# Performance work log

Measured on AMD Instinct MI355X. Metric: run time of the kernel, lower is better.

## Reference

```python
import jax, jax.numpy as jnp
import numpy as np

HIDDEN = 512


def setup_inputs() -> dict:
    key = jax.random.key(0)
    k_x, k_ih, k_hh = jax.random.split(key, 3)
    B, T, I, H = 128, 1000, 2, HIDDEN
    x = jax.random.uniform(k_x, (B, T, I), dtype=jnp.float32)
    s_ih = 1.0 / np.sqrt(I)
    s_hh = 1.0 / np.sqrt(H)
    weight_ih = jax.random.normal(k_ih, (I, 4 * H), dtype=jnp.float32) * s_ih
    weight_hh = jax.random.normal(k_hh, (H, 4 * H), dtype=jnp.float32) * s_hh
    bias = jnp.zeros((4 * H,), dtype=jnp.float32)
    return {"x": x, "weight_ih": weight_ih, "weight_hh": weight_hh, "bias": bias}


def _lstm(x, weight_ih, weight_hh, bias):
    # x: [B, T, I] (batch_first) -> scan over time
    B, T, I = x.shape
    H = weight_hh.shape[0]
    # Precompute input contribution for all timesteps: [T, B, 4H]
    x_t = jnp.transpose(x, (1, 0, 2))
    xW = jnp.einsum('tbi,ih->tbh', x_t, weight_ih) + bias

    def step(carry, xw_t):
        h0, c0 = carry
        gates = h0 @ weight_hh + xw_t  # [B, 4H]
        f, i, o, g = jnp.split(gates, 4, axis=1)
        c1 = jax.nn.sigmoid(f) * c0 + jax.nn.sigmoid(i) * jnp.tanh(g)
        h1 = jax.nn.sigmoid(o) * jnp.tanh(c1)
        return (h1, c1), (h1, c1)

    h0 = jnp.zeros((B, H), dtype=x.dtype)
    c0 = jnp.zeros((B, H), dtype=x.dtype)
    _, (h_n, c_n) = jax.lax.scan(step, (h0, c0), xW)
    # [T, B, H] -> [B, T, H] (batch_first)
    return jnp.transpose(h_n, (1, 0, 2)), jnp.transpose(c_n, (1, 0, 2))


def reference(x, weight_ih, weight_hh, bias):
    return _lstm(x, weight_ih, weight_hh, bias)
```

## Files before the change

### kernel.cpp

```cpp
#include <hip/hip_runtime.h>

#define TT 1000
#define HH 512
#define G4 2048
#define NG 32
#define SLOTS 8
#define SPG 4
#define HCBLK 64

typedef __attribute__((ext_vector_type(8))) short bf16x8;
typedef __attribute__((ext_vector_type(4))) float f32x4;

__device__ __forceinline__ float sigm(float v) { return 1.0f / (1.0f + __expf(-v)); }
__device__ __forceinline__ float tanh_fast(float v) { return 2.0f / (1.0f + __expf(-2.0f * v)) - 1.0f; }

__device__ __forceinline__ unsigned short bf16rne(float f) {
    unsigned u = __float_as_uint(f);
    return (unsigned short)((u + 0x7fffu + ((u >> 16) & 1u)) >> 16);
}

__global__ __launch_bounds__(512, 1)
void lstm_bo(const float* __restrict__ x,
             const float* __restrict__ wih,
             const float* __restrict__ whh,
             const float* __restrict__ bias,
             float* __restrict__ out,
             float* ws)
{
    __shared__ unsigned long long ldsA[2][4][132];

    const int bid  = blockIdx.x;
    const int g    = bid & (NG - 1);
    const int slot = bid >> 5;
    const int tid  = threadIdx.x;
    const int wv   = tid >> 6;
    const int lane = tid & 63;
    const int col  = lane & 15;
    const int kb   = lane >> 4;
    const int q    = col & 3;
    const int q1   = q & 1, q2 = q >> 1;
    const int cc   = col >> 2;
    const int hc0  = slot * HCBLK + wv * 8 + cc;
    const int hc1  = hc0 + 4;

    unsigned long long* slab = (unsigned long long*)ws;
    unsigned* flags = (unsigned*)((char*)ws + 256 * 1024);

    for (int i = tid; i < 2 * 4 * 132; i += 512)
        ((unsigned long long*)ldsA)[i] = 0ULL;

    const int gc0 = q * 512 + hc0;
    const int gc1 = q * 512 + hc1;
    bf16x8 breg0[16], breg1[16];
    #pragma unroll
    for (int kt = 0; kt < 16; ++kt) {
        bf16x8 f0, f1;
        #pragma unroll
        for (int j = 0; j < 8; ++j) {
            int k = kt * 32 + kb * 8 + j;
            f0[j] = (short)bf16rne(whh[(size_t)k * G4 + gc0]);
            f1[j] = (short)bf16rne(whh[(size_t)k * G4 + gc1]);
        }
        breg0[kt] = f0;
        breg1[kt] = f1;
    }

    float wA0[4], wB0[4], bb0[4], wA1[4], wB1[4], bb1[4];
    #pragma unroll
    for (int j = 0; j < 4; ++j) {
        int a0 = j * 512 + hc0, a1 = j * 512 + hc1;
        wA0[j] = wih[a0]; wB0[j] = wih[G4 + a0]; bb0[j] = bias[a0];
        wA1[j] = wih[a1]; wB1[j] = wih[G4 + a1]; bb1[j] = bias[a1];
    }

    float cst0 = 0.0f, cst1 = 0.0f;
    const size_t OSZ = (size_t)128 * TT * HH;
    const int bSel = g * SPG + q;
    const float* xp = x + (size_t)bSel * TT * 2;
    float2 xv = *(const float2*)(xp);
    const bool storer = (kb == 0) && (cc == 0);

    const int crow = tid >> 7;
    const int ck   = tid & 127;

    __syncthreads();

    for (int t = 0; t < TT; ++t) {
        const int rb = t & 1;

        f32x4 acc0 = {0.f, 0.f, 0.f, 0.f};
        f32x4 acc1 = {0.f, 0.f, 0.f, 0.f};
        #pragma unroll
        for (int kt = 0; kt < 16; ++kt) {
            bf16x8 a = {0, 0, 0, 0, 0, 0, 0, 0};
            if (col < 4)
                a = *(const bf16x8*)&ldsA[rb][col][(kt * 8 + kb * 2) ^ (2 * col)];
            acc0 = __builtin_amdgcn_mfma_f32_16x16x32_bf16(a, breg0[kt], acc0, 0, 0, 0);
            acc1 = __builtin_amdgcn_mfma_f32_16x16x32_bf16(a, breg1[kt], acc1, 0, 0, 0);
        }

        float h1a, c1a;
        {
            float v0 = acc0[0], v1 = acc0[1], v2 = acc0[2], v3 = acc0[3];
            float vq = q2 ? (q1 ? v3 : v2) : (q1 ? v1 : v0);
            float s1 = q2 ? (q1 ? v2 : v3) : (q1 ? v0 : v1);
            float s2 = q2 ? (q1 ? v1 : v0) : (q1 ? v3 : v2);
            float s3 = q2 ? (q1 ? v0 : v1) : (q1 ? v2 : v3);
            float g1 = __shfl_xor(s1, 1);
            float g2 = __shfl_xor(s2, 2);
            float g3 = __shfl_xor(s3, 3);
            float fv = q2 ? (q1 ? g3 : g2) : (q1 ? g1 : vq);
            float iv = q2 ? (q1 ? g2 : g3) : (q1 ? vq : g1);
            float ov = q2 ? (q1 ? g1 : vq) : (q1 ? g3 : g2);
            float gv = q2 ? (q1 ? vq : g1) : (q1 ? g2 : g3);
            fv += xv.x * wA0[0] + xv.y * wB0[0] + bb0[0];
            iv += xv.x * wA0[1] + xv.y * wB0[1] + bb0[1];
            ov += xv.x * wA0[2] + xv.y * wB0[2] + bb0[2];
            gv += xv.x * wA0[3] + xv.y * wB0[3] + bb0[3];
            c1a = sigm(fv) * cst0 + sigm(iv) * tanh_fast(gv);
            h1a = sigm(ov) * tanh_fast(c1a);
            cst0 = c1a;
        }
        float h1b, c1b;
        {
            float v0 = acc1[0], v1 = acc1[1], v2 = acc1[2], v3 = acc1[3];
            float vq = q2 ? (q1 ? v3 : v2) : (q1 ? v1 : v0);
            float s1 = q2 ? (q1 ? v2 : v3) : (q1 ? v0 : v1);
            float s2 = q2 ? (q1 ? v1 : v0) : (q1 ? v3 : v2);
            float s3 = q2 ? (q1 ? v0 : v1) : (q1 ? v2 : v3);
            float g1 = __shfl_xor(s1, 1);
            float g2 = __shfl_xor(s2, 2);
            float g3 = __shfl_xor(s3, 3);
            float fv = q2 ? (q1 ? g3 : g2) : (q1 ? g1 : vq);
            float iv = q2 ? (q1 ? g2 : g3) : (q1 ? vq : g1);
            float ov = q2 ? (q1 ? g1 : vq) : (q1 ? g3 : g2);
            float gv = q2 ? (q1 ? vq : g1) : (q1 ? g2 : g3);
            fv += xv.x * wA1[0] + xv.y * wB1[0] + bb1[0];
            iv += xv.x * wA1[1] + xv.y * wB1[1] + bb1[1];
            ov += xv.x * wA1[2] + xv.y * wB1[2] + bb1[2];
            gv += xv.x * wA1[3] + xv.y * wB1[3] + bb1[3];
            c1b = sigm(fv) * cst1 + sigm(iv) * tanh_fast(gv);
            h1b = sigm(ov) * tanh_fast(c1b);
            cst1 = c1b;
        }

        float ha1 = __shfl_xor(h1a, 4), ha2 = __shfl_xor(h1a, 8), ha3 = __shfl_xor(ha1, 8);
        float hb1 = __shfl_xor(h1b, 4), hb2 = __shfl_xor(h1b, 8), hb3 = __shfl_xor(hb1, 8);
        float ca1 = __shfl_xor(c1a, 4), ca2 = __shfl_xor(c1a, 8), ca3 = __shfl_xor(ca1, 8);
        float cb1 = __shfl_xor(c1b, 4), cb2 = __shfl_xor(c1b, 8), cb3 = __shfl_xor(cb1, 8);

        const unsigned tag = (unsigned)(t + 1);
        const int phase = (t + 1) & 1;

        if (t + 1 < TT) {
            if (storer) {
                unsigned long long w0 =
                      (unsigned long long)bf16rne(h1a)
                    | ((unsigned long long)bf16rne(ha1) << 16)
                    | ((unsigned long long)bf16rne(ha2) << 32)
                    | ((unsigned long long)bf16rne(ha3) << 48);
                unsigned long long w1 =
                      (unsigned long long)bf16rne(h1b)
                    | ((unsigned long long)bf16rne(hb1) << 16)
                    | ((unsigned long long)bf16rne(hb2) << 32)
                    | ((unsigned long long)bf16rne(hb3) << 48);
                unsigned long long* dst = slab
                    + ((size_t)(phase * 128 + bSel)) * 128 + slot * 16 + wv * 2;
                __hip_atomic_store(dst,     w0, __ATOMIC_RELAXED, __HIP_MEMORY_SCOPE_AGENT);
                __hip_atomic_store(dst + 1, w1, __ATOMIC_RELAXED, __HIP_MEMORY_SCOPE_AGENT);
            }

            asm volatile("s_waitcnt vmcnt(0)" ::: "memory");
            asm volatile("s_barrier" ::: "memory");

            if (tid == 0)
                __hip_atomic_store(&flags[(g * SLOTS + slot) * 16], tag,
                                   __ATOMIC_RELAXED, __HIP_MEMORY_SCOPE_AGENT);

            if (storer) {
                size_t oidx = ((size_t)bSel * TT + t) * HH + slot * HCBLK + wv * 8;
                float4 hq0 = {h1a, ha1, ha2, ha3};
                float4 cq0 = {c1a, ca1, ca2, ca3};
                float4 hq1 = {h1b, hb1, hb2, hb3};
                float4 cq1 = {c1b, cb1, cb2, cb3};
                *(float4*)(out + oidx) = hq0;
                *(float4*)(out + oidx + 4) = hq1;
                *(float4*)(out + OSZ + oidx) = cq0;
                *(float4*)(out + OSZ + oidx + 4) = cq1;
            }

            xv = *(const float2*)(xp + 2 * (t + 1));

            if (wv == 0) {
                long gd = 0;
                for (;;) {
                    unsigned fl = (lane < SLOTS)
                        ? __hip_atomic_load(&flags[(g * SLOTS + lane) * 16],
                                            __ATOMIC_RELAXED, __HIP_MEMORY_SCOPE_AGENT)
                        : tag;
                    if (__all(fl >= tag)) break;
                    __builtin_amdgcn_s_sleep(1);
                    if (++gd > 20000000L) break;
                }
            }
            asm volatile("s_barrier" ::: "memory");

            const unsigned long long* myp = slab
                + ((size_t)(phase * 128 + g * SPG + crow)) * 128 + ck;
            unsigned long long d = __hip_atomic_load(myp, __ATOMIC_RELAXED,
                                                     __HIP_MEMORY_SCOPE_AGENT);
            ldsA[phase][crow][ck ^ (2 * crow)] = d;

            asm volatile("s_waitcnt lgkmcnt(0)\n\ts_barrier" ::: "memory");
        } else {
            if (storer) {
                size_t oidx = ((size_t)bSel * TT + t) * HH + slot * HCBLK + wv * 8;
                float4 hq0 = {h1a, ha1, ha2, ha3};
                float4 cq0 = {c1a, ca1, ca2, ca3};
                float4 hq1 = {h1b, hb1, hb2, hb3};
                float4 cq1 = {c1b, cb1, cb2, cb3};
                *(float4*)(out + oidx) = hq0;
                *(float4*)(out + oidx + 4) = hq1;
                *(float4*)(out + OSZ + oidx) = cq0;
                *(float4*)(out + OSZ + oidx + 4) = cq1;
            }
        }
    }
}

extern "C" void kernel_launch(void* const* d_in, const int* in_sizes, int n_in,
                              void* d_out, int out_size, void* d_ws, size_t ws_size,
                              hipStream_t stream) {
    const float* x    = (const float*)d_in[0];
    const float* wih  = (const float*)d_in[1];
    const float* whh  = (const float*)d_in[2];
    const float* bias = (const float*)d_in[3];
    float* out = (float*)d_out;
    float* ws  = (float*)d_ws;

    hipMemsetAsync((char*)d_ws + 256 * 1024, 0, NG * SLOTS * 16 * sizeof(unsigned), stream);

    dim3 grid(NG * SLOTS), block(512);
    hipLaunchKernelGGL(lstm_bo, grid, block, 0, stream, x, wih, whh, bias, out, ws);
}
```

Measured before the change: 3.275 ms.

## Interleave two independent batch chains per block to hide sync latency

```diff
diff --git a/kernel.cpp b/kernel.cpp
--- a/kernel.cpp
+++ b/kernel.cpp
@@ -3,9 +3,8 @@
 #define TT 1000
 #define HH 512
 #define G4 2048
-#define NG 32
 #define SLOTS 8
-#define SPG 4
+#define SPG 2
 #define HCBLK 64
 
 typedef __attribute__((ext_vector_type(8))) short bf16x8;
@@ -19,19 +18,91 @@
     return (unsigned short)((u + 0x7fffu + ((u >> 16) & 1u)) >> 16);
 }
 
+#define CHAIN_STEP(ROWS, XV, CST0, CST1, HQ0, HQ1, CQ0, CQ1) do {              \
+    f32x4 acc0 = {0.f, 0.f, 0.f, 0.f};                                         \
+    f32x4 acc1 = {0.f, 0.f, 0.f, 0.f};                                         \
+    _Pragma("unroll")                                                          \
+    for (int kt = 0; kt < 16; ++kt) {                                          \
+        bf16x8 a = {0, 0, 0, 0, 0, 0, 0, 0};                                   \
+        if (col < 2)                                                           \
+            a = *(const bf16x8*)&(ROWS)[col][(kt * 8 + kb * 2) ^ (2 * col)];   \
+        acc0 = __builtin_amdgcn_mfma_f32_16x16x32_bf16(a, breg0[kt], acc0, 0, 0, 0); \
+        acc1 = __builtin_amdgcn_mfma_f32_16x16x32_bf16(a, breg1[kt], acc1, 0, 0, 0); \
+    }                                                                          \
+    float h1a, c1a;                                                            \
+    {                                                                          \
+        float v0 = acc0[0], v1 = acc0[1], v2 = acc0[2], v3 = acc0[3];          \
+        float vq = q2 ? (q1 ? v3 : v2) : (q1 ? v1 : v0);                       \
+        float s1 = q2 ? (q1 ? v2 : v3) : (q1 ? v0 : v1);                       \
+        float s2 = q2 ? (q1 ? v1 : v0) : (q1 ? v3 : v2);                       \
+        float s3 = q2 ? (q1 ? v0 : v1) : (q1 ? v2 : v3);                       \
+        float g1 = __shfl_xor(s1, 1);                                          \
+        float g2 = __shfl_xor(s2, 2);                                          \
+        float g3 = __shfl_xor(s3, 3);                                          \
+        float fv = q2 ? (q1 ? g3 : g2) : (q1 ? g1 : vq);                       \
+        float iv = q2 ? (q1 ? g2 : g3) : (q1 ? vq : g1);                       \
+        float ov = q2 ? (q1 ? g1 : vq) : (q1 ? g3 : g2);                       \
+        float gv = q2 ? (q1 ? vq : g1) : (q1 ? g2 : g3);                       \
+        fv += (XV).x * wA0[0] + (XV).y * wB0[0] + bb0[0];                      \
+        iv += (XV).x * wA0[1] + (XV).y * wB0[1] + bb0[1];                      \
+        ov += (XV).x * wA0[2] + (XV).y * wB0[2] + bb0[2];                      \
+        gv += (XV).x * wA0[3] + (XV).y * wB0[3] + bb0[3];                      \
+        c1a = sigm(fv) * (CST0) + sigm(iv) * tanh_fast(gv);                    \
+        h1a = sigm(ov) * tanh_fast(c1a);                                       \
+        (CST0) = c1a;                                                          \
+    }                                                                          \
+    float h1b, c1b;                                                            \
+    {                                                                          \
+        float v0 = acc1[0], v1 = acc1[1], v2 = acc1[2], v3 = acc1[3];          \
+        float vq = q2 ? (q1 ? v3 : v2) : (q1 ? v1 : v0);                       \
+        float s1 = q2 ? (q1 ? v2 : v3) : (q1 ? v0 : v1);                       \
+        float s2 = q2 ? (q1 ? v1 : v0) : (q1 ? v3 : v2);                       \
+        float s3 = q2 ? (q1 ? v0 : v1) : (q1 ? v2 : v3);                       \
+        float g1 = __shfl_xor(s1, 1);                                          \
+        float g2 = __shfl_xor(s2, 2);                                          \
+        float g3 = __shfl_xor(s3, 3);                                          \
+        float fv = q2 ? (q1 ? g3 : g2) : (q1 ? g1 : vq);                       \
+        float iv = q2 ? (q1 ? g2 : g3) : (q1 ? vq : g1);                       \
+        float ov = q2 ? (q1 ? g1 : vq) : (q1 ? g3 : g2);                       \
+        float gv = q2 ? (q1 ? vq : g1) : (q1 ? g2 : g3);                       \
+        fv += (XV).x * wA1[0] + (XV).y * wB1[0] + bb1[0];                      \
+        iv += (XV).x * wA1[1] + (XV).y * wB1[1] + bb1[1];                      \
+        ov += (XV).x * wA1[2] + (XV).y * wB1[2] + bb1[2];                      \
+        gv += (XV).x * wA1[3] + (XV).y * wB1[3] + bb1[3];                      \
+        c1b = sigm(fv) * (CST1) + sigm(iv) * tanh_fast(gv);                    \
+        h1b = sigm(ov) * tanh_fast(c1b);                                       \
+        (CST1) = c1b;                                                          \
+    }                                                                          \
+    {                                                                          \
+        float ha1 = __shfl_xor(h1a, 4), ha2 = __shfl_xor(h1a, 8);              \
+        float ha3 = __shfl_xor(ha1, 8);                                        \
+        float hb1 = __shfl_xor(h1b, 4), hb2 = __shfl_xor(h1b, 8);              \
+        float hb3 = __shfl_xor(hb1, 8);                                        \
+        float ca1 = __shfl_xor(c1a, 4), ca2 = __shfl_xor(c1a, 8);              \
+        float ca3 = __shfl_xor(ca1, 8);                                        \
+        float cb1 = __shfl_xor(c1b, 4), cb2 = __shfl_xor(c1b, 8);              \
+        float cb3 = __shfl_xor(cb1, 8);                                        \
+        (HQ0) = (float4){h1a, ha1, ha2, ha3};                                  \
+        (HQ1) = (float4){h1b, hb1, hb2, hb3};                                  \
+        (CQ0) = (float4){c1a, ca1, ca2, ca3};                                  \
+        (CQ1) = (float4){c1b, cb1, cb2, cb3};                                  \
+    }                                                                          \
+} while (0)
+
 __global__ __launch_bounds__(512, 1)
-void lstm_bo(const float* __restrict__ x,
+void lstm_2c(const float* __restrict__ x,
              const float* __restrict__ wih,
              const float* __restrict__ whh,
              const float* __restrict__ bias,
              float* __restrict__ out,
              float* ws)
 {
-    __shared__ unsigned long long ldsA[2][4][132];
+    __shared__ unsigned long long ldsA[2][2][2][132];
 
     const int bid  = blockIdx.x;
-    const int g    = bid & (NG - 1);
+    const int gA   = bid & 31;
     const int slot = bid >> 5;
+    const int gB   = gA + 32;
     const int tid  = threadIdx.x;
     const int wv   = tid >> 6;
     const int lane = tid & 63;
@@ -42,11 +113,16 @@
     const int cc   = col >> 2;
     const int hc0  = slot * HCBLK + wv * 8 + cc;
     const int hc1  = hc0 + 4;
+    const int rowSel = kb * 4 + q;
+    const int row2 = rowSel & 1;
+    const int bA   = gA * SPG + row2;
+    const int bB   = gB * SPG + row2;
+    const bool storer = (kb == 0) && (cc == 0) && (q < 2);
 
     unsigned long long* slab = (unsigned long long*)ws;
     unsigned* flags = (unsigned*)((char*)ws + 256 * 1024);
 
-    for (int i = tid; i < 2 * 4 * 132; i += 512)
+    for (int i = tid; i < 2 * 2 * 2 * 132; i += 512)
         ((unsigned long long*)ldsA)[i] = 0ULL;
 
     const int gc0 = q * 512 + hc0;
@@ -73,156 +149,123 @@
         wA1[j] = wih[a1]; wB1[j] = wih[G4 + a1]; bb1[j] = bias[a1];
     }
 
-    float cst0 = 0.0f, cst1 = 0.0f;
+    float cstA0 = 0.f, cstA1 = 0.f, cstB0 = 0.f, cstB1 = 0.f;
     const size_t OSZ = (size_t)128 * TT * HH;
-    const int bSel = g * SPG + q;
-    const float* xp = x + (size_t)bSel * TT * 2;
-    float2 xv = *(const float2*)(xp);
-    const bool storer = (kb == 0) && (cc == 0);
-
-    const int crow = tid >> 7;
+    const float* xpA = x + (size_t)bA * TT * 2;
+    const float* xpB = x + (size_t)bB * TT * 2;
+    float2 xvA = *(const float2*)(xpA);
+    float2 xvB = *(const float2*)(xpB);
+
+    const int rch  = tid >> 8;
+    const int crow = (tid >> 7) & 1;
     const int ck   = tid & 127;
+    const int srcRow = (rch == 0 ? gA : gB) * SPG + crow;
 
     __syncthreads();
 
     for (int t = 0; t < TT; ++t) {
         const int rb = t & 1;
-
-        f32x4 acc0 = {0.f, 0.f, 0.f, 0.f};
-        f32x4 acc1 = {0.f, 0.f, 0.f, 0.f};
-        #pragma unroll
-        for (int kt = 0; kt < 16; ++kt) {
-            bf16x8 a = {0, 0, 0, 0, 0, 0, 0, 0};
-            if (col < 4)
-                a = *(const bf16x8*)&ldsA[rb][col][(kt * 8 + kb * 2) ^ (2 * col)];
-            acc0 = __builtin_amdgcn_mfma_f32_16x16x32_bf16(a, breg0[kt], acc0, 0, 0, 0);
-            acc1 = __builtin_amdgcn_mfma_f32_16x16x32_bf16(a, breg1[kt], acc1, 0, 0, 0);
-        }
-
-        float h1a, c1a;
-        {
-            float v0 = acc0[0], v1 = acc0[1], v2 = acc0[2], v3 = acc0[3];
-            float vq = q2 ? (q1 ? v3 : v2) : (q1 ? v1 : v0);
-            float s1 = q2 ? (q1 ? v2 : v3) : (q1 ? v0 : v1);
-            float s2 = q2 ? (q1 ? v1 : v0) : (q1 ? v3 : v2);
-            float s3 = q2 ? (q1 ? v0 : v1) : (q1 ? v2 : v3);
-            float g1 = __shfl_xor(s1, 1);
-            float g2 = __shfl_xor(s2, 2);
-            float g3 = __shfl_xor(s3, 3);
-            float fv = q2 ? (q1 ? g3 : g2) : (q1 ? g1 : vq);
-            float iv = q2 ? (q1 ? g2 : g3) : (q1 ? vq : g1);
-            float ov = q2 ? (q1 ? g1 : vq) : (q1 ? g3 : g2);
-            float gv = q2 ? (q1 ? vq : g1) : (q1 ? g2 : g3);
-            fv += xv.x * wA0[0] + xv.y * wB0[0] + bb0[0];
-            iv += xv.x * wA0[1] + xv.y * wB0[1] + bb0[1];
-            ov += xv.x * wA0[2] + xv.y * wB0[2] + bb0[2];
-            gv += xv.x * wA0[3] + xv.y * wB0[3] + bb0[3];
-            c1a = sigm(fv) * cst0 + sigm(iv) * tanh_fast(gv);
-            h1a = sigm(ov) * tanh_fast(c1a);
-            cst0 = c1a;
-        }
-        float h1b, c1b;
-        {
-            float v0 = acc1[0], v1 = acc1[1], v2 = acc1[2], v3 = acc1[3];
-            float vq = q2 ? (q1 ? v3 : v2) : (q1 ? v1 : v0);
-            float s1 = q2 ? (q1 ? v2 : v3) : (q1 ? v0 : v1);
-            float s2 = q2 ? (q1 ? v1 : v0) : (q1 ? v3 : v2);
-            float s3 = q2 ? (q1 ? v0 : v1) : (q1 ? v2 : v3);
-            float g1 = __shfl_xor(s1, 1);
-            float g2 = __shfl_xor(s2, 2);
-            float g3 = __shfl_xor(s3, 3);
-            float fv = q2 ? (q1 ? g3 : g2) : (q1 ? g1 : vq);
-            float iv = q2 ? (q1 ? g2 : g3) : (q1 ? vq : g1);
-            float ov = q2 ? (q1 ? g1 : vq) : (q1 ? g3 : g2);
-            float gv = q2 ? (q1 ? vq : g1) : (q1 ? g2 : g3);
-            fv += xv.x * wA1[0] + xv.y * wB1[0] + bb1[0];
-            iv += xv.x * wA1[1] + xv.y * wB1[1] + bb1[1];
-            ov += xv.x * wA1[2] + xv.y * wB1[2] + bb1[2];
-            gv += xv.x * wA1[3] + xv.y * wB1[3] + bb1[3];
-            c1b = sigm(fv) * cst1 + sigm(iv) * tanh_fast(gv);
-            h1b = sigm(ov) * tanh_fast(c1b);
-            cst1 = c1b;
-        }
-
-        float ha1 = __shfl_xor(h1a, 4), ha2 = __shfl_xor(h1a, 8), ha3 = __shfl_xor(ha1, 8);
-        float hb1 = __shfl_xor(h1b, 4), hb2 = __shfl_xor(h1b, 8), hb3 = __shfl_xor(hb1, 8);
-        float ca1 = __shfl_xor(c1a, 4), ca2 = __shfl_xor(c1a, 8), ca3 = __shfl_xor(ca1, 8);
-        float cb1 = __shfl_xor(c1b, 4), cb2 = __shfl_xor(c1b, 8), cb3 = __shfl_xor(cb1, 8);
-
         const unsigned tag = (unsigned)(t + 1);
         const int phase = (t + 1) & 1;
+        float4 hqA0, hqA1, cqA0, cqA1, hqB0, hqB1, cqB0, cqB1;
+
+        CHAIN_STEP(ldsA[0][rb], xvA, cstA0, cstA1, hqA0, hqA1, cqA0, cqA1);
+        if (t + 1 < TT && storer) {
+            unsigned long long w0 =
+                  (unsigned long long)bf16rne(hqA0.x)
+                | ((unsigned long long)bf16rne(hqA0.y) << 16)
+                | ((unsigned long long)bf16rne(hqA0.z) << 32)
+                | ((unsigned long long)bf16rne(hqA0.w) << 48);
+            unsigned long long w1 =
+                  (unsigned long long)bf16rne(hqA1.x)
+                | ((unsigned long long)bf16rne(hqA1.y) << 16)
+                | ((unsigned long long)bf16rne(hqA1.z) << 32)
+                | ((unsigned long long)bf16rne(hqA1.w) << 48);
+            unsigned long long* dst = slab
+                + ((size_t)(phase * 128 + bA)) * 128 + slot * 16 + wv * 2;
+            __hip_atomic_store(dst,     w0, __ATOMIC_RELAXED, __HIP_MEMORY_SCOPE_AGENT);
+            __hip_atomic_store(dst + 1, w1, __ATOMIC_RELAXED, __HIP_MEMORY_SCOPE_AGENT);
+        }
+
+        CHAIN_STEP(ldsA[1][rb], xvB, cstB0, cstB1, hqB0, hqB1, cqB0, cqB1);
+        if (t + 1 < TT && storer) {
+            unsigned long long w0 =
+                  (unsigned long long)bf16rne(hqB0.x)
+                | ((unsigned long long)bf16rne(hqB0.y) << 16)
+                | ((unsigned long long)bf16rne(hqB0.z) << 32)
+                | ((unsigned long long)bf16rne(hqB0.w) << 48);
+            unsigned long long w1 =
+                  (unsigned long long)bf16rne(hqB1.x)
+                | ((unsigned long long)bf16rne(hqB1.y) << 16)
+                | ((unsigned long long)bf16rne(hqB1.z) << 32)
+                | ((unsigned long long)bf16rne(hqB1.w) << 48);
+            unsigned long long* dst = slab
+                + ((size_t)(phase * 128 + bB)) * 128 + slot * 16 + wv * 2;
+            __hip_atomic_store(dst,     w0, __ATOMIC_RELAXED, __HIP_MEMORY_SCOPE_AGENT);
+            __hip_atomic_store(dst + 1, w1, __ATOMIC_RELAXED, __HIP_MEMORY_SCOPE_AGENT);
+        }
 
         if (t + 1 < TT) {
-            if (storer) {
-                unsigned long long w0 =
-                      (unsigned long long)bf16rne(h1a)
-                    | ((unsigned long long)bf16rne(ha1) << 16)
-                    | ((unsigned long long)bf16rne(ha2) << 32)
-                    | ((unsigned long long)bf16rne(ha3) << 48);
-                unsigned long long w1 =
-                      (unsigned long long)bf16rne(h1b)
-                    | ((unsigned long long)bf16rne(hb1) << 16)
-                    | ((unsigned long long)bf16rne(hb2) << 32)
-                    | ((unsigned long long)bf16rne(hb3) << 48);
-                unsigned long long* dst = slab
-                    + ((size_t)(phase * 128 + bSel)) * 128 + slot * 16 + wv * 2;
-                __hip_atomic_store(dst,     w0, __ATOMIC_RELAXED, __HIP_MEMORY_SCOPE_AGENT);
-                __hip_atomic_store(dst + 1, w1, __ATOMIC_RELAXED, __HIP_MEMORY_SCOPE_AGENT);
-            }
-
             asm volatile("s_waitcnt vmcnt(0)" ::: "memory");
             asm volatile("s_barrier" ::: "memory");
 
-            if (tid == 0)
-                __hip_atomic_store(&flags[(g * SLOTS + slot) * 16], tag,
+            if (tid == 0) {
+                __hip_atomic_store(&flags[(gA * SLOTS + slot) * 16], tag,
                                    __ATOMIC_RELAXED, __HIP_MEMORY_SCOPE_AGENT);
+                __hip_atomic_store(&flags[(gB * SLOTS + slot) * 16], tag,
+                                   __ATOMIC_RELAXED, __HIP_MEMORY_SCOPE_AGENT);
+            }
 
             if (storer) {
-                size_t oidx = ((size_t)bSel * TT + t) * HH + slot * HCBLK + wv * 8;
-                float4 hq0 = {h1a, ha1, ha2, ha3};
-                float4 cq0 = {c1a, ca1, ca2, ca3};
-                float4 hq1 = {h1b, hb1, hb2, hb3};
-                float4 cq1 = {c1b, cb1, cb2, cb3};
-                *(float4*)(out + oidx) = hq0;
-                *(float4*)(out + oidx + 4) = hq1;
-                *(float4*)(out + OSZ + oidx) = cq0;
-                *(float4*)(out + OSZ + oidx + 4) = cq1;
-            }
-
-            xv = *(const float2*)(xp + 2 * (t + 1));
-
-            if (wv == 0) {
+                size_t oA = ((size_t)bA * TT + t) * HH + slot * HCBLK + wv * 8;
+                *(float4*)(out + oA)           = hqA0;
+                *(float4*)(out + oA + 4)       = hqA1;
+                *(float4*)(out + OSZ + oA)     = cqA0;
+                *(float4*)(out + OSZ + oA + 4) = cqA1;
+                size_t oB = ((size_t)bB * TT + t) * HH + slot * HCBLK + wv * 8;
+                *(float4*)(out + oB)           = hqB0;
+                *(float4*)(out + oB + 4)       = hqB1;
+                *(float4*)(out + OSZ + oB)     = cqB0;
+                *(float4*)(out + OSZ + oB + 4) = cqB1;
+            }
+
+            xvA = *(const float2*)(xpA + 2 * (t + 1));
+            xvB = *(const float2*)(xpB + 2 * (t + 1));
+
+            {
                 long gd = 0;
                 for (;;) {
-                    unsigned fl = (lane < SLOTS)
-                        ? __hip_atomic_load(&flags[(g * SLOTS + lane) * 16],
-                                            __ATOMIC_RELAXED, __HIP_MEMORY_SCOPE_AGENT)
-                        : tag;
+                    unsigned fl = tag;
+                    if (lane < 16) {
+                        int gx = (lane < 8) ? gA : gB;
+                        fl = __hip_atomic_load(&flags[(gx * SLOTS + (lane & 7)) * 16],
+                                               __ATOMIC_RELAXED, __HIP_MEMORY_SCOPE_AGENT);
+                    }
                     if (__all(fl >= tag)) break;
                     __builtin_amdgcn_s_sleep(1);
                     if (++gd > 20000000L) break;
                 }
             }
-            asm volatile("s_barrier" ::: "memory");
 
             const unsigned long long* myp = slab
-                + ((size_t)(phase * 128 + g * SPG + crow)) * 128 + ck;
+                + ((size_t)(phase * 128 + srcRow)) * 128 + ck;
             unsigned long long d = __hip_atomic_load(myp, __ATOMIC_RELAXED,
                                                      __HIP_MEMORY_SCOPE_AGENT);
-            ldsA[phase][crow][ck ^ (2 * crow)] = d;
+            ldsA[rch][phase][crow][ck ^ (2 * crow)] = d;
 
             asm volatile("s_waitcnt lgkmcnt(0)\n\ts_barrier" ::: "memory");
         } else {
             if (storer) {
-                size_t oidx = ((size_t)bSel * TT + t) * HH + slot * HCBLK + wv * 8;
-                float4 hq0 = {h1a, ha1, ha2, ha3};
-                float4 cq0 = {c1a, ca1, ca2, ca3};
-                float4 hq1 = {h1b, hb1, hb2, hb3};
-                float4 cq1 = {c1b, cb1, cb2, cb3};
-                *(float4*)(out + oidx) = hq0;
-                *(float4*)(out + oidx + 4) = hq1;
-                *(float4*)(out + OSZ + oidx) = cq0;
-                *(float4*)(out + OSZ + oidx + 4) = cq1;
+                size_t oA = ((size_t)bA * TT + t) * HH + slot * HCBLK + wv * 8;
+                *(float4*)(out + oA)           = hqA0;
+                *(float4*)(out + oA + 4)       = hqA1;
+                *(float4*)(out + OSZ + oA)     = cqA0;
+                *(float4*)(out + OSZ + oA + 4) = cqA1;
+                size_t oB = ((size_t)bB * TT + t) * HH + slot * HCBLK + wv * 8;
+                *(float4*)(out + oB)           = hqB0;
+                *(float4*)(out + oB + 4)       = hqB1;
+                *(float4*)(out + OSZ + oB)     = cqB0;
+                *(float4*)(out + OSZ + oB + 4) = cqB1;
             }
         }
     }
@@ -238,8 +281,8 @@
     float* out = (float*)d_out;
     float* ws  = (float*)d_ws;
 
-    hipMemsetAsync((char*)d_ws + 256 * 1024, 0, NG * SLOTS * 16 * sizeof(unsigned), stream);
-
-    dim3 grid(NG * SLOTS), block(512);
-    hipLaunchKernelGGL(lstm_bo, grid, block, 0, stream, x, wih, whh, bias, out, ws);
+    hipMemsetAsync((char*)d_ws + 256 * 1024, 0, 512 * 16 * sizeof(unsigned), stream);
+
+    dim3 grid(256), block(512);
+    hipLaunchKernelGGL(lstm_2c, grid, block, 0, stream, x, wih, whh, bias, out, ws);
 }
```

Result: slower. 5.392 ms (+64.7%).
